# Kernel tuning notes

Hardware: AMD Instinct MI355X
Metric: run time of the kernel (lower is better)

## Reference

```python
import jax, jax.numpy as jnp
import numpy as np
import math

# SLAYER SRM-alpha neuron / simulation constants (from netParams yaml)
THETA = 10.0     # spike threshold
TAU_SR = 10.0    # PSP (srm) kernel time constant
TAU_REF = 1.0    # refractory kernel time constant
SCALE_REF = 2.0  # refractory kernel scale
TS = 1.0         # simulation timestep
POOL_GAIN = 1.1 * THETA  # SLAYER pool: sum over window scaled by 1.1*theta

# alpha kernel eps(t) = (t/tau) * exp(1 - t/tau); at lag L*Ts this equals
# (e*Ts/tau) * L * d**L with d = exp(-Ts/tau). Convolution with it is computed
# by a fused two-state linear recurrence (lax.scan over time), matching the
# fused-scan structure of the original SLAYER CUDA kernels.

def psp(x):
    """Leaky temporal integration: x [..., T] -> psp [..., T]."""
    d = math.exp(-TS / TAU_SR)
    B = math.e * TS / TAU_SR
    xt = jnp.moveaxis(x, -1, 0)  # [T, ...]
    z = jnp.zeros_like(xt[0])
    def step(carry, xn):
        p, q = carry
        q = d * (q + p)          # q_n = sum_{m<n} x[m] (n-m) d^(n-m)
        p = d * p + xn           # p_n = sum_{m<=n} x[m] d^(n-m)
        return (p, q), B * q
    _, out = jax.lax.scan(step, (z, z), xt)
    return jnp.moveaxis(out, 0, -1)


def spike(u):
    """Threshold spike generation with refractory feedback (SRM).
    u [..., T] membrane drive -> binary spikes [..., T].
    Refractory kernel: -scaleRef*theta * (t/tauRef) * exp(1 - t/tauRef).
    """
    d = math.exp(-TS / TAU_REF)
    A = -SCALE_REF * THETA * math.e * TS / TAU_REF
    ut = jnp.moveaxis(u, -1, 0)
    z = jnp.zeros_like(ut[0])
    def surr(v):
        # hard threshold forward, sigmoid surrogate gradient (straight-through)
        hard = (v >= THETA).astype(v.dtype)
        soft = jax.nn.sigmoid((v - THETA) * (4.0 / THETA))
        return soft + jax.lax.stop_gradient(hard - soft)
    def step(carry, un):
        p, q = carry
        q = d * (q + p)
        s = surr(un + A * q)  # membrane = drive + refractory response
        p = d * p + s
        return (p, q), s
    _, out = jax.lax.scan(step, (z, z), ut)
    return jnp.moveaxis(out, 0, -1)


def conv_t(x, w, pad):
    """Per-timestep 2D conv on [N,C,H,W,T]; kernel w [O,I,kh,kw]."""
    return jax.lax.conv_general_dilated(
        x, w[..., None], window_strides=(1, 1, 1),
        padding=[(pad, pad), (pad, pad), (0, 0)],
        dimension_numbers=("NCHWT", "OIHWT", "NCHWT"))


def pool2(x):
    """SLAYER 2x2 sum-pool scaled by 1.1*theta, per timestep."""
    N, C, H, W, T = x.shape
    return x.reshape(N, C, H // 2, 2, W // 2, 2, T).sum(axis=(3, 5)) * POOL_GAIN


def dense_t(x, w):
    """Dense over (C,H,W) per timestep: x [N,C,H,W,T], w [O,C,H,W] -> [N,O,T]."""
    return jnp.einsum("nchwt,ochw->not", x, w)


def setup_inputs() -> dict:
    key = jax.random.key(0)
    k0, k1, k2, k3, k4 = jax.random.split(key, 5)
    spikeInput = (jax.random.uniform(k0, (8, 1, 30, 30, 300)) < 0.05).astype(jnp.float32)
    conv1_w = jax.random.normal(k1, (16, 1, 5, 5), jnp.float32) * 1.0
    conv2_w = jax.random.normal(k2, (32, 16, 3, 3), jnp.float32) * 0.5
    conv3_w = jax.random.normal(k3, (64, 32, 3, 3), jnp.float32) * 0.5
    fc1_w = jax.random.normal(k4, (10, 64, 7, 7), jnp.float32) * 0.5
    return {"spikeInput": spikeInput, "conv1_w": conv1_w, "conv2_w": conv2_w,
            "conv3_w": conv3_w, "fc1_w": fc1_w}


def reference(spikeInput, conv1_w, conv2_w, conv3_w, fc1_w):
    s1 = spike(conv_t(psp(spikeInput), conv1_w, pad=1))  # [8,16,28,28,300]
    s2 = spike(pool2(psp(s1)))                            # [8,16,14,14,300]
    s3 = spike(conv_t(psp(s2), conv2_w, pad=1))           # [8,32,14,14,300]
    s4 = spike(pool2(psp(s3)))                            # [8,32,7,7,300]
    s5 = spike(conv_t(psp(s4), conv3_w, pad=1))           # [8,64,7,7,300]
    out = spike(dense_t(psp(s5), fc1_w))                  # [8,10,300]
    return out
```

## Files before the change

### kernel.cpp

```cpp
#include <hip/hip_runtime.h>
#include <hip/hip_bf16.h>
#include <cstdint>

#define TT 300
#define NB 8

static constexpr float D_SR  = 0.90483741803595957f;
static constexpr float B_SR  = 0.27182818284590454f;
static constexpr float D_RF  = 0.36787944117144233f;
static constexpr float A_RF  = -54.365636569180902f;
static constexpr float THETA_F = 10.0f;
static constexpr float PGAIN = 11.0f;

typedef const float __attribute__((address_space(4)))* cfp;

__global__ void k_wtr(const float* __restrict__ w1, const float* __restrict__ w2,
                      const float* __restrict__ w3, float* __restrict__ t1,
                      float* __restrict__ t2, float* __restrict__ t3) {
    int g = blockIdx.x * blockDim.x + threadIdx.x;
    if (g < 400) {
        int oc = g / 25, s = g % 25;
        t1[s * 16 + oc] = w1[g];
    } else if (g < 400 + 4608) {
        int h = g - 400, oc = h / 144, s = h % 144;
        t2[s * 32 + oc] = w2[h];
    } else if (g < 400 + 4608 + 18432) {
        int h = g - 5008, oc = h / 288, s = h % 288;
        t3[s * 64 + oc] = w3[h];
    }
}

__global__ void k_psp_tr(const float* __restrict__ in, float* __restrict__ out, int NS) {
    int i = blockIdx.x * blockDim.x + threadIdx.x;
    if (i >= NS) return;
    const float4* x4 = (const float4*)(in + (size_t)i * TT);
    constexpr int G4 = 5, NG = TT / (4 * G4);
    float4 Aa[G4], Bb[G4];
    #pragma unroll
    for (int u = 0; u < G4; ++u) Aa[u] = x4[u];
    float p = 0.f, q = 0.f;
    for (int g = 0; g < NG; ++g) {
        if (g + 1 < NG) {
            #pragma unroll
            for (int u = 0; u < G4; ++u) Bb[u] = x4[(g + 1) * G4 + u];
        }
        int t0 = g * G4 * 4;
        #pragma unroll
        for (int u = 0; u < G4; ++u) {
            float xs[4] = {Aa[u].x, Aa[u].y, Aa[u].z, Aa[u].w};
            #pragma unroll
            for (int e = 0; e < 4; ++e) {
                q = D_SR * (q + p);
                p = D_SR * p + xs[e];
                out[(size_t)(t0 + u * 4 + e) * NS + i] = B_SR * q;
            }
        }
        #pragma unroll
        for (int u = 0; u < G4; ++u) Aa[u] = Bb[u];
    }
}

template<int CI, int CO, int KS, int HI, int WI, int HO, int WO, int OCW, int J>
__global__ __launch_bounds__(256) void k_conv(const float* __restrict__ in,
                                              const float* __restrict__ wT,
                                              float* __restrict__ out) {
    constexpr int PW = WI + 2, PH = HI + 2, PST = PH * PW;
    __shared__ float lds[CI * PST];
    const int tid = threadIdx.x;
    const int tn  = blockIdx.x;
    cfp wc = (cfp)(uintptr_t)wT;
    const float* img = in + (size_t)tn * (CI * HI * WI);
    for (int idx = tid; idx < CI * PST; idx += 256) lds[idx] = 0.f;
    __syncthreads();
    for (int idx = tid; idx < CI * HI * WI; idx += 256) {
        int ic = idx / (HI * WI), rem = idx % (HI * WI);
        int r = rem / WI, c = rem % WI;
        lds[ic * PST + (r + 1) * PW + (c + 1)] = img[idx];
    }
    __syncthreads();

    const int wave = __builtin_amdgcn_readfirstlane(tid >> 6);
    const int lane = tid & 63;
    const int l = lane < 49 ? lane : 48;
    const int oc0 = (CO == OCW) ? 0 : wave * OCW;

    int pbase[J];
    #pragma unroll
    for (int j = 0; j < J; ++j) {
        int g = (CO == OCW) ? (wave * J + j) : j;
        int px = g * 49 + l;
        pbase[j] = (px / WO) * PW + (px % WO);
    }
    float acc[J * OCW];
    #pragma unroll
    for (int a = 0; a < J * OCW; ++a) acc[a] = 0.f;

    for (int ic = 0; ic < CI; ++ic) {
        #pragma unroll
        for (int kh = 0; kh < KS; ++kh) {
            #pragma unroll
            for (int kw = 0; kw < KS; ++kw) {
                const int step = (ic * KS + kh) * KS + kw;
                float iv[J];
                #pragma unroll
                for (int j = 0; j < J; ++j)
                    iv[j] = lds[ic * PST + pbase[j] + kh * PW + kw];
                #pragma unroll
                for (int o = 0; o < OCW; ++o) {
                    float wv = wc[(size_t)step * CO + oc0 + o];
                    #pragma unroll
                    for (int j = 0; j < J; ++j) acc[j * OCW + o] += iv[j] * wv;
                }
            }
        }
    }
    if (lane < 49) {
        #pragma unroll
        for (int j = 0; j < J; ++j) {
            int g = (CO == OCW) ? (wave * J + j) : j;
            int px = g * 49 + lane;
            #pragma unroll
            for (int o = 0; o < OCW; ++o)
                out[((size_t)tn * CO + oc0 + o) * (HO * WO) + px] = acc[j * OCW + o];
        }
    }
}

template<int RB, int RE, int IRB, int IRE>
__device__ __forceinline__ void conv3_rows(const float* lds, const float* wp,
                                           float* __restrict__ out, int tn, int lane) {
    constexpr int NR = RE - RB;
    float acc[NR * 7];
    #pragma unroll
    for (int a = 0; a < NR * 7; ++a) acc[a] = 0.f;
    for (int ic = 0; ic < 32; ++ic) {
        float w[9];
        #pragma unroll
        for (int s = 0; s < 9; ++s) w[s] = wp[(ic * 9 + s) * 64];
        #pragma unroll
        for (int ir = IRB; ir < IRE; ++ir) {
            float row[7];
            #pragma unroll
            for (int c = 0; c < 7; ++c) row[c] = lds[ic * 49 + ir * 7 + c];
            #pragma unroll
            for (int kh = 0; kh < 3; ++kh) {
                const int r = ir + 1 - kh;
                if (r < RB || r >= RE) continue;
                #pragma unroll
                for (int c = 0; c < 7; ++c) {
                    #pragma unroll
                    for (int kw = 0; kw < 3; ++kw) {
                        const int jc = c + kw - 1;
                        if (jc < 0 || jc >= 7) continue;
                        acc[(r - RB) * 7 + c] += row[jc] * w[kh * 3 + kw];
                    }
                }
            }
        }
    }
    #pragma unroll
    for (int r = RB; r < RE; ++r)
        #pragma unroll
        for (int c = 0; c < 7; ++c)
            out[((size_t)tn * 64 + lane) * 49 + r * 7 + c] = acc[(r - RB) * 7 + c];
}

__global__ __launch_bounds__(128) void k_conv3(const float* __restrict__ in,
                                               const float* __restrict__ wT,
                                               float* __restrict__ out) {
    __shared__ float lds[1568];
    const int tid = threadIdx.x;
    const int tn  = blockIdx.x;
    const float4* src = (const float4*)(in + (size_t)tn * 1568);
    for (int idx = tid; idx < 392; idx += 128) ((float4*)lds)[idx] = src[idx];
    __syncthreads();
    const int lane = tid & 63;
    const float* wp = wT + lane;
    if (tid < 64) conv3_rows<0, 4, 0, 5>(lds, wp, out, tn, lane);
    else          conv3_rows<4, 7, 3, 7>(lds, wp, out, tn, lane);
}

template<int C, int HI, int WI>
__global__ void k_fuse_pool(const float* __restrict__ U, float* __restrict__ X) {
    constexpr int HO = HI / 2, WO = WI / 2;
    constexpr int M   = NB * C * HO * WO;
    constexpr int NSI = NB * C * HI * WI;
    int i = blockIdx.x * blockDim.x + threadIdx.x;
    if (i >= M) return;
    int j = i % WO, r = (i / WO) % HO, nc = i / (WO * HO);
    size_t base = (size_t)(nc * HI + 2 * r) * WI + 2 * j;
    const float2* R0 = (const float2*)(U + base);
    const float2* R1 = (const float2*)(U + base + WI);
    constexpr int G = 10, NG = TT / G;
    float2 A0[G], A1[G], B0[G], B1[G];
    #pragma unroll
    for (int u = 0; u < G; ++u) {
        A0[u] = R0[(size_t)u * (NSI / 2)];
        A1[u] = R1[(size_t)u * (NSI / 2)];
    }
    float p00=0,q00=0,p01=0,q01=0,p10=0,q10=0,p11=0,q11=0;
    float P=0,Q=0, sp=0,sq=0, P2=0,Q2=0;
    for (int g = 0; g < NG; ++g) {
        if (g + 1 < NG) {
            #pragma unroll
            for (int u = 0; u < G; ++u) {
                B0[u] = R0[(size_t)((g + 1) * G + u) * (NSI / 2)];
                B1[u] = R1[(size_t)((g + 1) * G + u) * (NSI / 2)];
            }
        }
        #pragma unroll
        for (int u = 0; u < G; ++u) {
            int t = g * G + u;
            float s0, s1, s2, s3;
            q00 = D_RF*(q00+p00); { float v = A0[u].x + A_RF*q00; s0 = (v>=THETA_F)?1.f:0.f; } p00 = D_RF*p00+s0;
            q01 = D_RF*(q01+p01); { float v = A0[u].y + A_RF*q01; s1 = (v>=THETA_F)?1.f:0.f; } p01 = D_RF*p01+s1;
            q10 = D_RF*(q10+p10); { float v = A1[u].x + A_RF*q10; s2 = (v>=THETA_F)?1.f:0.f; } p10 = D_RF*p10+s2;
            q11 = D_RF*(q11+p11); { float v = A1[u].y + A_RF*q11; s3 = (v>=THETA_F)?1.f:0.f; } p11 = D_RF*p11+s3;
            float x = (s0 + s1 + s2 + s3) * PGAIN;
            Q = D_SR*(Q+P); P = D_SR*P + x; float drive = B_SR*Q;
            sq = D_RF*(sq+sp); float v2 = drive + A_RF*sq; float sv = (v2>=THETA_F)?1.f:0.f; sp = D_RF*sp+sv;
            Q2 = D_SR*(Q2+P2); P2 = D_SR*P2 + sv;
            X[(size_t)t * M + i] = B_SR * Q2;
        }
        #pragma unroll
        for (int u = 0; u < G; ++u) { A0[u] = B0[u]; A1[u] = B1[u]; }
    }
}

__global__ void k_spike_psp(const float* __restrict__ U, float* __restrict__ X, int NS) {
    int i = blockIdx.x * blockDim.x + threadIdx.x;
    if (i >= NS) return;
    constexpr int G = 20, NG = TT / G;
    float Aa[G], Bb[G];
    #pragma unroll
    for (int u = 0; u < G; ++u) Aa[u] = U[(size_t)u * NS + i];
    float p = 0, q = 0, P = 0, Q = 0;
    for (int g = 0; g < NG; ++g) {
        if (g + 1 < NG) {
            #pragma unroll
            for (int u = 0; u < G; ++u) Bb[u] = U[(size_t)((g + 1) * G + u) * NS + i];
        }
        #pragma unroll
        for (int u = 0; u < G; ++u) {
            int t = g * G + u;
            q = D_RF * (q + p);
            float v = Aa[u] + A_RF * q;
            float s = (v >= THETA_F) ? 1.f : 0.f;
            p = D_RF * p + s;
            Q = D_SR * (Q + P); P = D_SR * P + s;
            X[(size_t)t * NS + i] = B_SR * Q;
        }
        #pragma unroll
        for (int u = 0; u < G; ++u) Aa[u] = Bb[u];
    }
}

__global__ void k_dense(const float* __restrict__ X, const float* __restrict__ wf,
                        float* __restrict__ G_) {
    int tn = blockIdx.x;
    int lane = threadIdx.x;
    const float* xb = X + (size_t)tn * 3136;
    float acc[10];
    #pragma unroll
    for (int o = 0; o < 10; ++o) acc[o] = 0.f;
    for (int it = 0; it < 49; ++it) {
        int k = it * 64 + lane;
        float xv = xb[k];
        #pragma unroll
        for (int o = 0; o < 10; ++o) acc[o] += xv * wf[o * 3136 + k];
    }
    #pragma unroll
    for (int off = 32; off > 0; off >>= 1) {
        #pragma unroll
        for (int o = 0; o < 10; ++o) acc[o] += __shfl_down(acc[o], off);
    }
    if (lane == 0) {
        #pragma unroll
        for (int o = 0; o < 10; ++o) G_[tn * 10 + o] = acc[o];
    }
}

__global__ void k_spike_out(const float* __restrict__ G_, float* __restrict__ out) {
    int i = threadIdx.x;
    if (i >= 80) return;
    constexpr int G = 20, NG = TT / G;
    float Aa[G], Bb[G];
    #pragma unroll
    for (int u = 0; u < G; ++u) Aa[u] = G_[u * 80 + i];
    float p = 0, q = 0;
    for (int g = 0; g < NG; ++g) {
        if (g + 1 < NG) {
            #pragma unroll
            for (int u = 0; u < G; ++u) Bb[u] = G_[((g + 1) * G + u) * 80 + i];
        }
        #pragma unroll
        for (int u = 0; u < G; ++u) {
            int t = g * G + u;
            q = D_RF * (q + p);
            float v = Aa[u] + A_RF * q;
            float s = (v >= THETA_F) ? 1.f : 0.f;
            p = D_RF * p + s;
            out[(size_t)i * TT + t] = s;
        }
        #pragma unroll
        for (int u = 0; u < G; ++u) Aa[u] = Bb[u];
    }
}

static inline int cdiv(int a, int b) { return (a + b - 1) / b; }

extern "C" void kernel_launch(void* const* d_in, const int* in_sizes, int n_in,
                              void* d_out, int out_size, void* d_ws, size_t ws_size,
                              hipStream_t stream) {
    const float* x  = (const float*)d_in[0];
    const float* w1 = (const float*)d_in[1];
    const float* w2 = (const float*)d_in[2];
    const float* w3 = (const float*)d_in[3];
    const float* wf = (const float*)d_in[4];
    float* out = (float*)d_out;
    float* ws  = (float*)d_ws;

    float* A   = ws;
    float* U1  = ws + 2160000;
    float* X2  = ws + 32265600;
    float* Gg  = ws + 39792000;
    float* wT1 = ws + 39816000;
    float* wT2 = ws + 39816400;
    float* wT3 = ws + 39821008;
    float* U2  = U1;
    float* X4  = U1 + 16000000;
    float* U3  = X2;
    float* X5  = U1;

    const int B = 256;
    k_wtr<<<cdiv(23440, B), B, 0, stream>>>(w1, w2, w3, wT1, wT2, wT3);
    k_psp_tr<<<cdiv(7200, B), B, 0, stream>>>(x, A, 7200);
    k_conv<1, 16, 5, 30, 30, 28, 28, 16, 4><<<2400, B, 0, stream>>>(A, wT1, U1);
    k_fuse_pool<16, 28, 28><<<cdiv(25088, B), B, 0, stream>>>(U1, X2);
    k_conv<16, 32, 3, 14, 14, 14, 14, 32, 1><<<2400, B, 0, stream>>>(X2, wT2, U2);
    k_fuse_pool<32, 14, 14><<<cdiv(12544, B), B, 0, stream>>>(U2, X4);
    k_conv3<<<2400, 128, 0, stream>>>(X4, wT3, U3);
    k_spike_psp<<<cdiv(25088, B), B, 0, stream>>>(U3, X5, 25088);
    k_dense<<<2400, 64, 0, stream>>>(X5, wf, Gg);
    k_spike_out<<<1, 128, 0, stream>>>(Gg, out);
}
```

Baseline: 381.5 us.

## Add dedicated conv2 kernel with per-lane output channel and row-band register tiling

Replaces the generic conv kernel for layer 2 with a specialized kernel that handles two timestep-images per block. The inputs go into LDS as padded rows that are read with float4 loads. Each lane owns one output channel and accumulates a band of rows in registers, so weights are reused across all 14 columns. Results are staged back through LDS in two halves so the global stores are coalesced. This cuts redundant LDS and weight loads per FMA, at the cost of high register use (56 accumulators), an uneven row split between waves, and extra synchronisation.

```diff
diff --git a/kernel.cpp b/kernel.cpp
--- a/kernel.cpp
+++ b/kernel.cpp
@@ -126,6 +126,96 @@
     }
 }
 
+template<int R0, int R1>
+__device__ __forceinline__ void conv2_acc(const float* __restrict__ ib,
+                                          const float* __restrict__ wp,
+                                          float* __restrict__ acc) {
+    #pragma unroll
+    for (int a = 0; a < (R1 - R0) * 14; ++a) acc[a] = 0.f;
+    for (int ic = 0; ic < 16; ++ic) {
+        float w[9];
+        #pragma unroll
+        for (int s = 0; s < 9; ++s) w[s] = wp[(ic * 9 + s) * 32];
+        constexpr int IR0 = (R0 == 0) ? 0 : R0 - 1;
+        constexpr int IR1 = (R1 == 14) ? 13 : R1;
+        #pragma unroll
+        for (int ir = IR0; ir <= IR1; ++ir) {
+            const float4* rp = (const float4*)(ib + ic * 224 + ir * 16);
+            float4 a4 = rp[0], b4 = rp[1], c4 = rp[2], d4 = rp[3];
+            float row[14] = {a4.x, a4.y, a4.z, a4.w, b4.x, b4.y, b4.z, b4.w,
+                             c4.x, c4.y, c4.z, c4.w, d4.x, d4.y};
+            #pragma unroll
+            for (int kh = 0; kh < 3; ++kh) {
+                const int r = ir + 1 - kh;
+                if (r < R0 || r >= R1) continue;
+                #pragma unroll
+                for (int c = 0; c < 14; ++c) {
+                    #pragma unroll
+                    for (int kw = 0; kw < 3; ++kw) {
+                        const int jc = c + kw - 1;
+                        if (jc < 0 || jc >= 14) continue;
+                        acc[(r - R0) * 14 + c] += row[jc] * w[kh * 3 + kw];
+                    }
+                }
+            }
+        }
+    }
+}
+
+__global__ __launch_bounds__(256) void k_conv2(const float* __restrict__ in,
+                                               const float* __restrict__ wT,
+                                               float* __restrict__ out) {
+    __shared__ float lds[7168];
+    const int tid = threadIdx.x;
+    const int tn0 = blockIdx.x * 2;
+    const float* src = in + (size_t)tn0 * 3136;
+    for (int idx = tid; idx < 6272; idx += 256) {
+        int img = idx / 3136, rem = idx % 3136;
+        int ic = rem / 196, k = rem % 196;
+        int r = k / 14, c = k % 14;
+        lds[img * 3584 + ic * 224 + r * 16 + c] = src[idx];
+    }
+    __syncthreads();
+    const int wave = __builtin_amdgcn_readfirstlane(tid >> 6);
+    const int lane = tid & 63;
+    const int imgh = lane >> 5;
+    const int oc   = lane & 31;
+    const float* ib = lds + imgh * 3584;
+    const float* wp = wT + oc;
+    float acc[56];
+    if      (wave == 0) conv2_acc<0, 4 >(ib, wp, acc);
+    else if (wave == 1) conv2_acc<4, 7 >(ib, wp, acc);
+    else if (wave == 2) conv2_acc<7, 11>(ib, wp, acc);
+    else                conv2_acc<11, 14>(ib, wp, acc);
+    __syncthreads();
+    const int tb = (imgh * 32 + oc) * 99;
+    if (wave == 0) {
+        #pragma unroll
+        for (int j = 0; j < 56; ++j) lds[tb + j] = acc[j];
+    } else if (wave == 1) {
+        #pragma unroll
+        for (int j = 0; j < 42; ++j) lds[tb + 56 + j] = acc[j];
+    }
+    __syncthreads();
+    for (int idx = tid; idx < 6272; idx += 256) {
+        int img = idx / 3136, rem = idx % 3136, o = rem / 98, px = rem % 98;
+        out[((size_t)(tn0 + img) * 32 + o) * 196 + px] = lds[(img * 32 + o) * 99 + px];
+    }
+    __syncthreads();
+    if (wave == 2) {
+        #pragma unroll
+        for (int j = 0; j < 56; ++j) lds[tb + j] = acc[j];
+    } else if (wave == 3) {
+        #pragma unroll
+        for (int j = 0; j < 42; ++j) lds[tb + 56 + j] = acc[j];
+    }
+    __syncthreads();
+    for (int idx = tid; idx < 6272; idx += 256) {
+        int img = idx / 3136, rem = idx % 3136, o = rem / 98, px = rem % 98;
+        out[((size_t)(tn0 + img) * 32 + o) * 196 + 98 + px] = lds[(img * 32 + o) * 99 + px];
+    }
+}
+
 template<int RB, int RE, int IRB, int IRE>
 __device__ __forceinline__ void conv3_rows(const float* lds, const float* wp,
                                            float* __restrict__ out, int tn, int lane) {
@@ -337,7 +427,7 @@
     k_psp_tr<<<cdiv(7200, B), B, 0, stream>>>(x, A, 7200);
     k_conv<1, 16, 5, 30, 30, 28, 28, 16, 4><<<2400, B, 0, stream>>>(A, wT1, U1);
     k_fuse_pool<16, 28, 28><<<cdiv(25088, B), B, 0, stream>>>(U1, X2);
-    k_conv<16, 32, 3, 14, 14, 14, 14, 32, 1><<<2400, B, 0, stream>>>(X2, wT2, U2);
+    k_conv2<<<1200, B, 0, stream>>>(X2, wT2, U2);
     k_fuse_pool<32, 14, 14><<<cdiv(12544, B), B, 0, stream>>>(U2, X4);
     k_conv3<<<2400, 128, 0, stream>>>(X4, wT3, U3);
     k_spike_psp<<<cdiv(25088, B), B, 0, stream>>>(U3, X5, 25088);
```

New measurement: 395.5 us. 1.04x slower.

## Pad conv3 input and output rows for aligned float4 loads and stores

Applied to the files above, without the earlier changes.

The second pool stage now writes its output with each 7-wide row padded to 8 floats, so conv3 can read each input row as two float4 values. Conv3 also writes its output with each channel padded to 52 floats, which lets every thread issue vectorized float4 stores. Downstream, spike_psp runs over the padded element count and the dense kernel remaps its indices to skip the padding. In exchange, the padded buffers add memory traffic and some redundant spike_psp work on the padding elements.

```diff
diff --git a/kernel.cpp b/kernel.cpp
--- a/kernel.cpp
+++ b/kernel.cpp
@@ -126,9 +126,9 @@
     }
 }
 
-template<int RB, int RE, int IRB, int IRE>
-__device__ __forceinline__ void conv3_rows(const float* lds, const float* wp,
-                                           float* __restrict__ out, int tn, int lane) {
+template<int RB, int RE, int IRB, int IRE, int NV>
+__device__ __forceinline__ void conv3_rows(const float4* ib, const float* wp,
+                                           float* __restrict__ outb) {
     constexpr int NR = RE - RB;
     float acc[NR * 7];
     #pragma unroll
@@ -139,9 +139,9 @@
         for (int s = 0; s < 9; ++s) w[s] = wp[(ic * 9 + s) * 64];
         #pragma unroll
         for (int ir = IRB; ir < IRE; ++ir) {
-            float row[7];
-            #pragma unroll
-            for (int c = 0; c < 7; ++c) row[c] = lds[ic * 49 + ir * 7 + c];
+            float4 a4 = ib[ic * 14 + ir * 2];
+            float4 b4 = ib[ic * 14 + ir * 2 + 1];
+            float row[7] = {a4.x, a4.y, a4.z, a4.w, b4.x, b4.y, b4.z};
             #pragma unroll
             for (int kh = 0; kh < 3; ++kh) {
                 const int r = ir + 1 - kh;
@@ -158,36 +158,43 @@
             }
         }
     }
-    #pragma unroll
-    for (int r = RB; r < RE; ++r)
-        #pragma unroll
-        for (int c = 0; c < 7; ++c)
-            out[((size_t)tn * 64 + lane) * 49 + r * 7 + c] = acc[(r - RB) * 7 + c];
+    float4* o4 = (float4*)(outb + RB * 7);
+    #pragma unroll
+    for (int v = 0; v < NV; ++v) {
+        float x0 = (v * 4 + 0 < NR * 7) ? acc[v * 4 + 0] : 0.f;
+        float x1 = (v * 4 + 1 < NR * 7) ? acc[v * 4 + 1] : 0.f;
+        float x2 = (v * 4 + 2 < NR * 7) ? acc[v * 4 + 2] : 0.f;
+        float x3 = (v * 4 + 3 < NR * 7) ? acc[v * 4 + 3] : 0.f;
+        o4[v] = make_float4(x0, x1, x2, x3);
+    }
 }
 
 __global__ __launch_bounds__(128) void k_conv3(const float* __restrict__ in,
                                                const float* __restrict__ wT,
                                                float* __restrict__ out) {
-    __shared__ float lds[1568];
+    __shared__ float4 lds4[448];
     const int tid = threadIdx.x;
     const int tn  = blockIdx.x;
-    const float4* src = (const float4*)(in + (size_t)tn * 1568);
-    for (int idx = tid; idx < 392; idx += 128) ((float4*)lds)[idx] = src[idx];
+    const float4* src = (const float4*)(in + (size_t)tn * 1792);
+    for (int e = tid; e < 448; e += 128) lds4[e] = src[e];
     __syncthreads();
     const int lane = tid & 63;
     const float* wp = wT + lane;
-    if (tid < 64) conv3_rows<0, 4, 0, 5>(lds, wp, out, tn, lane);
-    else          conv3_rows<4, 7, 3, 7>(lds, wp, out, tn, lane);
-}
-
-template<int C, int HI, int WI>
+    float* outb = out + ((size_t)tn * 64 + lane) * 52;
+    if (tid < 64) conv3_rows<0, 4, 0, 5, 7>(lds4, wp, outb);
+    else          conv3_rows<4, 7, 3, 7, 6>(lds4, wp, outb);
+}
+
+template<int C, int HI, int WI, int WPAD>
 __global__ void k_fuse_pool(const float* __restrict__ U, float* __restrict__ X) {
     constexpr int HO = HI / 2, WO = WI / 2;
     constexpr int M   = NB * C * HO * WO;
+    constexpr int MO  = NB * C * HO * WPAD;
     constexpr int NSI = NB * C * HI * WI;
     int i = blockIdx.x * blockDim.x + threadIdx.x;
     if (i >= M) return;
     int j = i % WO, r = (i / WO) % HO, nc = i / (WO * HO);
+    const int oidx = nc * (HO * WPAD) + r * WPAD + j;
     size_t base = (size_t)(nc * HI + 2 * r) * WI + 2 * j;
     const float2* R0 = (const float2*)(U + base);
     const float2* R1 = (const float2*)(U + base + WI);
@@ -220,7 +227,7 @@
             Q = D_SR*(Q+P); P = D_SR*P + x; float drive = B_SR*Q;
             sq = D_RF*(sq+sp); float v2 = drive + A_RF*sq; float sv = (v2>=THETA_F)?1.f:0.f; sp = D_RF*sp+sv;
             Q2 = D_SR*(Q2+P2); P2 = D_SR*P2 + sv;
-            X[(size_t)t * M + i] = B_SR * Q2;
+            X[(size_t)t * MO + oidx] = B_SR * Q2;
         }
         #pragma unroll
         for (int u = 0; u < G; ++u) { A0[u] = B0[u]; A1[u] = B1[u]; }
@@ -259,15 +266,17 @@
                         float* __restrict__ G_) {
     int tn = blockIdx.x;
     int lane = threadIdx.x;
-    const float* xb = X + (size_t)tn * 3136;
+    int t = tn >> 3, n = tn & 7;
+    const float* xb = X + (size_t)t * 26624 + n * 3328;
     float acc[10];
     #pragma unroll
     for (int o = 0; o < 10; ++o) acc[o] = 0.f;
     for (int it = 0; it < 49; ++it) {
-        int k = it * 64 + lane;
-        float xv = xb[k];
-        #pragma unroll
-        for (int o = 0; o < 10; ++o) acc[o] += xv * wf[o * 3136 + k];
+        int j = it * 64 + lane;
+        int ic = j / 49, px = j - ic * 49;
+        float xv = xb[ic * 52 + px];
+        #pragma unroll
+        for (int o = 0; o < 10; ++o) acc[o] += xv * wf[o * 3136 + j];
     }
     #pragma unroll
     for (int off = 32; off > 0; off >>= 1) {
@@ -320,27 +329,28 @@
     float* out = (float*)d_out;
     float* ws  = (float*)d_ws;
 
-    float* A   = ws;
-    float* U1  = ws + 2160000;
-    float* X2  = ws + 32265600;
-    float* Gg  = ws + 39792000;
-    float* wT1 = ws + 39816000;
-    float* wT2 = ws + 39816400;
-    float* wT3 = ws + 39821008;
-    float* U2  = U1;
-    float* X4  = U1 + 16000000;
-    float* U3  = X2;
-    float* X5  = U1;
+    float* A    = ws;
+    float* U1   = ws + 2160000;
+    float* SLT2 = ws + 32265600;
+    float* Gg   = ws + 40252800;
+    float* wT1  = ws + 40276800;
+    float* wT2  = ws + 40277200;
+    float* wT3  = ws + 40281808;
+    float* X2   = SLT2;
+    float* U2   = U1;
+    float* X4   = U1 + 16000000;
+    float* U3   = SLT2;
+    float* X5   = U1;
 
     const int B = 256;
     k_wtr<<<cdiv(23440, B), B, 0, stream>>>(w1, w2, w3, wT1, wT2, wT3);
     k_psp_tr<<<cdiv(7200, B), B, 0, stream>>>(x, A, 7200);
     k_conv<1, 16, 5, 30, 30, 28, 28, 16, 4><<<2400, B, 0, stream>>>(A, wT1, U1);
-    k_fuse_pool<16, 28, 28><<<cdiv(25088, B), B, 0, stream>>>(U1, X2);
+    k_fuse_pool<16, 28, 28, 14><<<cdiv(25088, B), B, 0, stream>>>(U1, X2);
     k_conv<16, 32, 3, 14, 14, 14, 14, 32, 1><<<2400, B, 0, stream>>>(X2, wT2, U2);
-    k_fuse_pool<32, 14, 14><<<cdiv(12544, B), B, 0, stream>>>(U2, X4);
+    k_fuse_pool<32, 14, 14, 8><<<cdiv(12544, B), B, 0, stream>>>(U2, X4);
     k_conv3<<<2400, 128, 0, stream>>>(X4, wT3, U3);
-    k_spike_psp<<<cdiv(25088, B), B, 0, stream>>>(U3, X5, 25088);
+    k_spike_psp<<<cdiv(26624, B), B, 0, stream>>>(U3, X5, 26624);
     k_dense<<<2400, 64, 0, stream>>>(X5, wf, Gg);
     k_spike_out<<<1, 128, 0, stream>>>(Gg, out);
 }
```

New measurement: 395.4 us. 3.6% more time.
